# Kernel optimization log

Hardware: AMD Instinct MI355X
Metric: run time of the kernel (lower is better)

## Reference

```python
import jax, jax.numpy as jnp
import numpy as np

ATTENTION_DIM = 256
TEMPERATURE = 1.0
NEG_INF = -2.0**32 + 1.0  # matches tf code's padding value


def setup_inputs() -> dict:
    key = jax.random.key(0)
    k1, k2, k3, k4, k5, k6, k7 = jax.random.split(key, 7)
    B, Q, M, QD, MD, AD, VD = 8, 2048, 2048, 512, 512, 256, 256
    inputs = jax.random.normal(k1, (B, Q, QD), dtype=jnp.float32)
    memory = jax.random.normal(k2, (B, M, MD), dtype=jnp.float32)
    memory_lengths = jnp.maximum(jax.random.randint(k3, (B,), 0, M + 1), 1).astype(jnp.int32)
    query_lengths = jnp.maximum(jax.random.randint(k4, (B,), 0, Q + 1), 1).astype(jnp.int32)
    s = 0.02
    Wq = jax.random.normal(k5, (QD, AD), dtype=jnp.float32) * s
    Wk = jax.random.normal(k6, (MD, AD), dtype=jnp.float32) * s
    Wv = jax.random.normal(k7, (MD, VD), dtype=jnp.float32) * s
    return {"inputs": inputs, "memory": memory, "memory_lengths": memory_lengths,
            "query_lengths": query_lengths, "Wq": Wq, "Wk": Wk, "Wv": Wv}


def reference(inputs, memory, memory_lengths, query_lengths, Wq, Wk, Wv):
    # Dense projections (no bias). NOTE: original code (faithfully reproduced)
    # computes values with the KEY layer; Wv is unused.
    queries = jnp.einsum('bqd,da->bqa', inputs, Wq)   # [B,Q,AD]
    keys = jnp.einsum('bmd,da->bma', memory, Wk)      # [B,M,AD]
    values = jnp.einsum('bmd,da->bma', memory, Wk)    # [B,M,AD] (bug in source)

    logits = jnp.einsum('bqa,bma->bqm', queries, keys)
    logits = logits / jnp.sqrt(jnp.float32(ATTENTION_DIM)) / TEMPERATURE

    B, Q, _ = inputs.shape
    M = memory.shape[1]
    mem_mask = jnp.arange(M)[None, :] < memory_lengths[:, None]   # [B,M]
    qry_mask = jnp.arange(Q)[None, :] < query_lengths[:, None]    # [B,Q]
    length_mask = qry_mask[:, :, None] & mem_mask[:, None, :]     # [B,Q,M]

    logits = jnp.where(length_mask, logits, jnp.float32(NEG_INF))
    alignments = jax.nn.softmax(logits, axis=2)                   # [B,Q,M]
    contexts = jnp.einsum('bqm,bma->bqa', alignments, values)     # [B,Q,AD]
    return contexts, alignments
```

## Files before the change

### kernel.cpp

```cpp
#include <hip/hip_runtime.h>
#include <hip/hip_bf16.h>

typedef __attribute__((ext_vector_type(8))) short s8v;
typedef __attribute__((ext_vector_type(4))) float f4v;
typedef __attribute__((ext_vector_type(4))) unsigned short us4;
typedef unsigned short u16;

__device__ __forceinline__ u16 f2bf(float f) {
  union { float f; unsigned int u; } x;
  x.f = f;
  unsigned int lsb = (x.u >> 16) & 1u;
  return (u16)((x.u + 0x7fffu + lsb) >> 16);
}

__device__ __forceinline__ uint4 pack8(float4 a, float4 b) {
  union { u16 u[8]; uint4 v; } t;
  t.u[0] = f2bf(a.x); t.u[1] = f2bf(a.y); t.u[2] = f2bf(a.z); t.u[3] = f2bf(a.w);
  t.u[4] = f2bf(b.x); t.u[5] = f2bf(b.y); t.u[6] = f2bf(b.z); t.u[7] = f2bf(b.w);
  return t.v;
}

__global__ __launch_bounds__(256) void proj_kernel(
    const float* __restrict__ inputs, const float* __restrict__ memory,
    const float* __restrict__ Wq, const float* __restrict__ Wk,
    u16* __restrict__ qb, u16* __restrict__ krow, u16* __restrict__ kcol)
{
  __shared__ u16 Wt[64 * 264];
  __shared__ u16 At[64 * 40];

  const int tid = threadIdx.x;
  const int w = tid >> 6;
  const int l = tid & 63;
  const int lr = l & 15;
  const int lh = l >> 4;
  const int rbase = blockIdx.x * 64;
  const int n0 = blockIdx.y * 64;
  const int src = blockIdx.z;
  const float* __restrict__ A  = src ? memory : inputs;
  const float* __restrict__ Wg = src ? Wk : Wq;

  f4v acc[4];
#pragma unroll
  for (int i = 0; i < 4; ++i) acc[i] = f4v{0.f, 0.f, 0.f, 0.f};

  for (int kh = 0; kh < 2; ++kh) {
    {
      const int kl = tid >> 3;
      const int nl = (tid & 7) * 8;
#pragma unroll
      for (int i = 0; i < 8; ++i) {
        const int k = kl + i * 32;
        const float* s = Wg + (size_t)(kh * 256 + k) * 256 + n0 + nl;
        float4 x0 = *(const float4*)s;
        float4 x1 = *(const float4*)(s + 4);
        Wt[(nl + 0) * 264 + k] = f2bf(x0.x);
        Wt[(nl + 1) * 264 + k] = f2bf(x0.y);
        Wt[(nl + 2) * 264 + k] = f2bf(x0.z);
        Wt[(nl + 3) * 264 + k] = f2bf(x0.w);
        Wt[(nl + 4) * 264 + k] = f2bf(x1.x);
        Wt[(nl + 5) * 264 + k] = f2bf(x1.y);
        Wt[(nl + 6) * 264 + k] = f2bf(x1.z);
        Wt[(nl + 7) * 264 + k] = f2bf(x1.w);
      }
    }
    __syncthreads();
    for (int ks = 0; ks < 8; ++ks) {
      {
        const int row = tid >> 2;
        const int kk = (tid & 3) * 8;
        const float* s = A + (size_t)(rbase + row) * 512 + kh * 256 + ks * 32 + kk;
        float4 x0 = *(const float4*)s;
        float4 x1 = *(const float4*)(s + 4);
        *(uint4*)&At[row * 40 + kk] = pack8(x0, x1);
      }
      __syncthreads();
      const s8v af = *(const s8v*)&At[(w * 16 + lr) * 40 + lh * 8];
#pragma unroll
      for (int nt = 0; nt < 4; ++nt) {
        const s8v bf = *(const s8v*)&Wt[(nt * 16 + lr) * 264 + ks * 32 + lh * 8];
        acc[nt] = __builtin_amdgcn_mfma_f32_16x16x32_bf16(af, bf, acc[nt], 0, 0, 0);
      }
      __syncthreads();
    }
  }

  u16* __restrict__ dst = src ? krow : qb;
#pragma unroll
  for (int nt = 0; nt < 4; ++nt) {
    const int col = n0 + nt * 16 + lr;
    const int R0 = rbase + w * 16 + lh * 4;
    u16 u0 = f2bf(acc[nt][0]);
    u16 u1 = f2bf(acc[nt][1]);
    u16 u2 = f2bf(acc[nt][2]);
    u16 u3 = f2bf(acc[nt][3]);
    dst[(size_t)(R0 + 0) * 256 + col] = u0;
    dst[(size_t)(R0 + 1) * 256 + col] = u1;
    dst[(size_t)(R0 + 2) * 256 + col] = u2;
    dst[(size_t)(R0 + 3) * 256 + col] = u3;
    if (src) {
      const int bb = R0 >> 11;
      const int mm = R0 & 2047;
      us4 pk;
      pk[0] = u0; pk[1] = u1; pk[2] = u2; pk[3] = u3;
      *(us4*)&kcol[((size_t)bb * 256 + col) * 2048 + mm] = pk;
    }
  }
}

__global__ __launch_bounds__(256) void attn_sum_kernel(
    const u16* __restrict__ qb, const u16* __restrict__ krow,
    const int* __restrict__ mlens, const int* __restrict__ qlens,
    float* __restrict__ psum_p)
{
  __shared__ u16 kr[32 * 264];

  const int tid = threadIdx.x;
  const int w = tid >> 6;
  const int l = tid & 63;
  const int lr = l & 15;
  const int lh = l >> 4;
  const int bid = blockIdx.x;
  const int b = bid & 7;
  const int q0 = ((bid >> 3) & 31) * 64;
  const int ms = bid >> 8;
  const int m_base = ms * 256;
  const int mlen = mlens[b];
  const int qlen = qlens[b];
  const int qrow0 = q0 + w * 16 + lh * 4;

  s8v qf[8];
  {
    const u16* qp = qb + ((size_t)b * 2048 + q0 + w * 16 + lr) * 256 + lh * 8;
#pragma unroll
    for (int s = 0; s < 8; ++s) qf[s] = *(const s8v*)(qp + s * 32);
  }

  float psum[4] = {0.f, 0.f, 0.f, 0.f};
  const float C2 = 0.09016844005556021f;

  for (int mo = 0; mo < 256; mo += 32) {
    const int m0 = m_base + mo;
#pragma unroll
    for (int i = 0; i < 4; ++i) {
      const int idx = i * 256 + tid;
      const int m = idx >> 5, G = idx & 31;
      uint4 v = *(const uint4*)(krow + (((size_t)b * 2048 + m0 + m) << 8) + G * 8);
      *(uint4*)&kr[m * 264 + G * 8] = v;
    }
    __syncthreads();

    f4v sacc[2];
    sacc[0] = f4v{0.f, 0.f, 0.f, 0.f};
    sacc[1] = f4v{0.f, 0.f, 0.f, 0.f};
#pragma unroll
    for (int s = 0; s < 8; ++s) {
#pragma unroll
      for (int f = 0; f < 2; ++f) {
        const s8v bf = *(const s8v*)&kr[(f * 16 + lr) * 264 + s * 32 + lh * 8];
        sacc[f] = __builtin_amdgcn_mfma_f32_16x16x32_bf16(qf[s], bf, sacc[f], 0, 0, 0);
      }
    }
#pragma unroll
    for (int f = 0; f < 2; ++f) {
      const int m = m0 + f * 16 + lr;
      const bool vm = m < mlen;
#pragma unroll
      for (int r = 0; r < 4; ++r) {
        float p = exp2f(sacc[f][r] * C2);
        if (!vm) p = 0.f;
        if (qrow0 + r >= qlen) p = 1.f;
        psum[r] += p;
      }
    }
    __syncthreads();
  }

#pragma unroll
  for (int r = 0; r < 4; ++r) {
    float v = psum[r];
    v += __shfl_xor(v, 1);
    v += __shfl_xor(v, 2);
    v += __shfl_xor(v, 4);
    v += __shfl_xor(v, 8);
    psum[r] = v;
  }
  if (lr == 0) {
#pragma unroll
    for (int r = 0; r < 4; ++r)
      psum_p[ms * 16384 + b * 2048 + qrow0 + r] = psum[r];
  }
}

__global__ __launch_bounds__(256) void attn_wr_kernel(
    const u16* __restrict__ qb, const u16* __restrict__ krow,
    const u16* __restrict__ kcol, const int* __restrict__ mlens,
    const int* __restrict__ qlens, const float* __restrict__ psum_p,
    float* __restrict__ out_align, float* __restrict__ out_ctx,
    float* __restrict__ octx_ws)
{
  __shared__ u16 kr[32 * 264];
  __shared__ u16 kc[256 * 40];
  __shared__ u16 pl[4 * 16 * 40];

  const int tid = threadIdx.x;
  const int w = tid >> 6;
  const int l = tid & 63;
  const int lr = l & 15;
  const int lh = l >> 4;
  const int bid = blockIdx.x;
  const int b = bid & 7;
  const int q0 = ((bid >> 3) & 31) * 64;
  const int mh = bid >> 8;
  const int mstart = (mh == 0) ? 0 : (mh == 1 ? 704 : 1376);
  const int ntile = (mh == 0) ? 22 : 21;
  const int mlen = mlens[b];
  const int qlen = qlens[b];
  const int qrow0 = q0 + w * 16 + lh * 4;

  s8v qf[8];
  {
    const u16* qp = qb + ((size_t)b * 2048 + q0 + w * 16 + lr) * 256 + lh * 8;
#pragma unroll
    for (int s = 0; s < 8; ++s) qf[s] = *(const s8v*)(qp + s * 32);
  }

  float inv[4];
#pragma unroll
  for (int r = 0; r < 4; ++r) {
    const int q = b * 2048 + qrow0 + r;
    float s = 0.f;
#pragma unroll
    for (int j = 0; j < 8; ++j) s += psum_p[j * 16384 + q];
    inv[r] = 1.0f / s;
  }

  f4v oacc[16];
#pragma unroll
  for (int i = 0; i < 16; ++i) oacc[i] = f4v{0.f, 0.f, 0.f, 0.f};

  const float C2 = 0.09016844005556021f;

  for (int t = 0; t < ntile; ++t) {
    const int m0 = mstart + t * 32;
#pragma unroll
    for (int i = 0; i < 4; ++i) {
      const int idx = i * 256 + tid;
      const int m = idx >> 5, G = idx & 31;
      uint4 v = *(const uint4*)(krow + (((size_t)b * 2048 + m0 + m) << 8) + G * 8);
      *(uint4*)&kr[m * 264 + G * 8] = v;
      const int a2 = idx >> 2, gm = idx & 3;
      uint4 v2 = *(const uint4*)(kcol + (((size_t)b * 256 + a2) << 11) + m0 + gm * 8);
      *(uint4*)&kc[a2 * 40 + gm * 8] = v2;
    }
    __syncthreads();

    f4v sacc[2];
    sacc[0] = f4v{0.f, 0.f, 0.f, 0.f};
    sacc[1] = f4v{0.f, 0.f, 0.f, 0.f};
#pragma unroll
    for (int s = 0; s < 8; ++s) {
#pragma unroll
      for (int f = 0; f < 2; ++f) {
        const s8v bf = *(const s8v*)&kr[(f * 16 + lr) * 264 + s * 32 + lh * 8];
        sacc[f] = __builtin_amdgcn_mfma_f32_16x16x32_bf16(qf[s], bf, sacc[f], 0, 0, 0);
      }
    }

#pragma unroll
    for (int f = 0; f < 2; ++f) {
      const int m = m0 + f * 16 + lr;
      const bool vm = m < mlen;
#pragma unroll
      for (int r = 0; r < 4; ++r) {
        const int q = qrow0 + r;
        float p = exp2f(sacc[f][r] * C2);
        if (!vm) p = 0.f;
        if (q >= qlen) p = 1.f;
        const float pn = p * inv[r];
        __builtin_nontemporal_store(pn, &out_align[((size_t)b * 2048 + q) * 2048 + m]);
        pl[w * 640 + (lh * 4 + r) * 40 + f * 16 + lr] = f2bf(pn);
      }
    }

    const s8v pa = *(const s8v*)&pl[w * 640 + lr * 40 + lh * 8];
#pragma unroll
    for (int at = 0; at < 16; ++at) {
      const s8v vf = *(const s8v*)&kc[(at * 16 + lr) * 40 + lh * 8];
      oacc[at] = __builtin_amdgcn_mfma_f32_16x16x32_bf16(pa, vf, oacc[at], 0, 0, 0);
    }
    __syncthreads();
  }

  float* __restrict__ dst = (mh == 0) ? out_ctx : (octx_ws + (size_t)(mh - 1) * 4194304);
#pragma unroll
  for (int at = 0; at < 16; ++at) {
    const int a = at * 16 + lr;
#pragma unroll
    for (int r = 0; r < 4; ++r) {
      __builtin_nontemporal_store(oacc[at][r],
          &dst[((size_t)b * 2048 + qrow0 + r) * 256 + a]);
    }
  }
}

__global__ __launch_bounds__(256) void combine_kernel(
    float* __restrict__ out_ctx, const float* __restrict__ octx_ws)
{
  const size_t i = (size_t)blockIdx.x * 256 + threadIdx.x;
  float4 a = ((const float4*)out_ctx)[i];
  float4 c0 = ((const float4*)octx_ws)[i];
  float4 c1 = ((const float4*)(octx_ws + 4194304))[i];
  a.x += c0.x + c1.x; a.y += c0.y + c1.y;
  a.z += c0.z + c1.z; a.w += c0.w + c1.w;
  ((float4*)out_ctx)[i] = a;
}

extern "C" void kernel_launch(void* const* d_in, const int* in_sizes, int n_in,
                              void* d_out, int out_size, void* d_ws, size_t ws_size,
                              hipStream_t stream) {
  const float* inputs = (const float*)d_in[0];
  const float* memory = (const float*)d_in[1];
  const int* mlens    = (const int*)d_in[2];
  const int* qlens    = (const int*)d_in[3];
  const float* Wq     = (const float*)d_in[4];
  const float* Wk     = (const float*)d_in[5];
  (void)in_sizes; (void)n_in; (void)out_size; (void)ws_size;

  u16* wsu = (u16*)d_ws;
  u16* qb   = wsu;
  u16* krow = wsu + 4194304;
  u16* kcol = wsu + 8388608;
  float* psum_p = (float*)(wsu + 12582912);
  float* octx_ws = (float*)(wsu + 12845056);

  float* out_ctx = (float*)d_out;
  float* out_align = out_ctx + 4194304;

  proj_kernel<<<dim3(256, 4, 2), dim3(256), 0, stream>>>(
      inputs, memory, Wq, Wk, qb, krow, kcol);
  attn_sum_kernel<<<dim3(2048), dim3(256), 0, stream>>>(
      qb, krow, mlens, qlens, psum_p);
  attn_wr_kernel<<<dim3(768), dim3(256), 0, stream>>>(
      qb, krow, kcol, mlens, qlens, psum_p, out_align, out_ctx, octx_ws);
  combine_kernel<<<dim3(4096), dim3(256), 0, stream>>>(out_ctx, octx_ws);
}
```

Before: 187.5 us.

## Process two query tiles per block to reuse staged K tiles

Both attention kernels now give each block 128 query rows, as two 64-row sub-tiles, so every K tile staged in LDS serves twice the queries. This halves the global-to-LDS traffic for K. The write kernel also changes its memory split from three uneven chunks to four equal 512-column chunks. The combine kernel therefore sums three partial context buffers instead of two. The cost is doubled register state per thread (Q fragments and output accumulators), which may lower occupancy, plus a larger workspace and more reduction traffic in combine.

After: 254.9 us. +35.9%, slower.

```diff
diff --git a/kernel.cpp b/kernel.cpp
--- a/kernel.cpp
+++ b/kernel.cpp
@@ -121,21 +121,25 @@
   const int lh = l >> 4;
   const int bid = blockIdx.x;
   const int b = bid & 7;
-  const int q0 = ((bid >> 3) & 31) * 64;
-  const int ms = bid >> 8;
+  const int q0 = ((bid >> 3) & 15) * 128;
+  const int ms = bid >> 7;
   const int m_base = ms * 256;
   const int mlen = mlens[b];
   const int qlen = qlens[b];
-  const int qrow0 = q0 + w * 16 + lh * 4;
-
-  s8v qf[8];
-  {
-    const u16* qp = qb + ((size_t)b * 2048 + q0 + w * 16 + lr) * 256 + lh * 8;
-#pragma unroll
-    for (int s = 0; s < 8; ++s) qf[s] = *(const s8v*)(qp + s * 32);
-  }
-
-  float psum[4] = {0.f, 0.f, 0.f, 0.f};
+
+  s8v qf[2][8];
+#pragma unroll
+  for (int qt = 0; qt < 2; ++qt) {
+    const u16* qp = qb + ((size_t)b * 2048 + q0 + qt * 64 + w * 16 + lr) * 256 + lh * 8;
+#pragma unroll
+    for (int s = 0; s < 8; ++s) qf[qt][s] = *(const s8v*)(qp + s * 32);
+  }
+
+  float psum[2][4];
+#pragma unroll
+  for (int qt = 0; qt < 2; ++qt)
+#pragma unroll
+    for (int r = 0; r < 4; ++r) psum[qt][r] = 0.f;
   const float C2 = 0.09016844005556021f;
 
   for (int mo = 0; mo < 256; mo += 32) {
@@ -149,45 +153,53 @@
     }
     __syncthreads();
 
-    f4v sacc[2];
-    sacc[0] = f4v{0.f, 0.f, 0.f, 0.f};
-    sacc[1] = f4v{0.f, 0.f, 0.f, 0.f};
-#pragma unroll
-    for (int s = 0; s < 8; ++s) {
+#pragma unroll
+    for (int qt = 0; qt < 2; ++qt) {
+      f4v sacc[2];
+      sacc[0] = f4v{0.f, 0.f, 0.f, 0.f};
+      sacc[1] = f4v{0.f, 0.f, 0.f, 0.f};
+#pragma unroll
+      for (int s = 0; s < 8; ++s) {
+#pragma unroll
+        for (int f = 0; f < 2; ++f) {
+          const s8v bf = *(const s8v*)&kr[(f * 16 + lr) * 264 + s * 32 + lh * 8];
+          sacc[f] = __builtin_amdgcn_mfma_f32_16x16x32_bf16(qf[qt][s], bf, sacc[f], 0, 0, 0);
+        }
+      }
+      const int qrow0 = q0 + qt * 64 + w * 16 + lh * 4;
 #pragma unroll
       for (int f = 0; f < 2; ++f) {
-        const s8v bf = *(const s8v*)&kr[(f * 16 + lr) * 264 + s * 32 + lh * 8];
-        sacc[f] = __builtin_amdgcn_mfma_f32_16x16x32_bf16(qf[s], bf, sacc[f], 0, 0, 0);
-      }
-    }
-#pragma unroll
-    for (int f = 0; f < 2; ++f) {
-      const int m = m0 + f * 16 + lr;
-      const bool vm = m < mlen;
-#pragma unroll
-      for (int r = 0; r < 4; ++r) {
-        float p = exp2f(sacc[f][r] * C2);
-        if (!vm) p = 0.f;
-        if (qrow0 + r >= qlen) p = 1.f;
-        psum[r] += p;
-      }
-    }
-    __syncthreads();
-  }
-
-#pragma unroll
-  for (int r = 0; r < 4; ++r) {
-    float v = psum[r];
-    v += __shfl_xor(v, 1);
-    v += __shfl_xor(v, 2);
-    v += __shfl_xor(v, 4);
-    v += __shfl_xor(v, 8);
-    psum[r] = v;
-  }
-  if (lr == 0) {
-#pragma unroll
-    for (int r = 0; r < 4; ++r)
-      psum_p[ms * 16384 + b * 2048 + qrow0 + r] = psum[r];
+        const int m = m0 + f * 16 + lr;
+        const bool vm = m < mlen;
+#pragma unroll
+        for (int r = 0; r < 4; ++r) {
+          float p = exp2f(sacc[f][r] * C2);
+          if (!vm) p = 0.f;
+          if (qrow0 + r >= qlen) p = 1.f;
+          psum[qt][r] += p;
+        }
+      }
+    }
+    __syncthreads();
+  }
+
+#pragma unroll
+  for (int qt = 0; qt < 2; ++qt) {
+#pragma unroll
+    for (int r = 0; r < 4; ++r) {
+      float v = psum[qt][r];
+      v += __shfl_xor(v, 1);
+      v += __shfl_xor(v, 2);
+      v += __shfl_xor(v, 4);
+      v += __shfl_xor(v, 8);
+      psum[qt][r] = v;
+    }
+    if (lr == 0) {
+      const int qrow0 = q0 + qt * 64 + w * 16 + lh * 4;
+#pragma unroll
+      for (int r = 0; r < 4; ++r)
+        psum_p[ms * 16384 + b * 2048 + qrow0 + r] = psum[qt][r];
+    }
   }
 }
 
@@ -209,39 +221,43 @@
   const int lh = l >> 4;
   const int bid = blockIdx.x;
   const int b = bid & 7;
-  const int q0 = ((bid >> 3) & 31) * 64;
-  const int mh = bid >> 8;
-  const int mstart = (mh == 0) ? 0 : (mh == 1 ? 704 : 1376);
-  const int ntile = (mh == 0) ? 22 : 21;
+  const int q0 = ((bid >> 3) & 15) * 128;
+  const int mh = bid >> 7;
+  const int m_base = mh * 512;
   const int mlen = mlens[b];
   const int qlen = qlens[b];
-  const int qrow0 = q0 + w * 16 + lh * 4;
-
-  s8v qf[8];
-  {
-    const u16* qp = qb + ((size_t)b * 2048 + q0 + w * 16 + lr) * 256 + lh * 8;
-#pragma unroll
-    for (int s = 0; s < 8; ++s) qf[s] = *(const s8v*)(qp + s * 32);
-  }
-
-  float inv[4];
-#pragma unroll
-  for (int r = 0; r < 4; ++r) {
-    const int q = b * 2048 + qrow0 + r;
-    float s = 0.f;
-#pragma unroll
-    for (int j = 0; j < 8; ++j) s += psum_p[j * 16384 + q];
-    inv[r] = 1.0f / s;
-  }
-
-  f4v oacc[16];
-#pragma unroll
-  for (int i = 0; i < 16; ++i) oacc[i] = f4v{0.f, 0.f, 0.f, 0.f};
+
+  s8v qf[2][8];
+#pragma unroll
+  for (int qt = 0; qt < 2; ++qt) {
+    const u16* qp = qb + ((size_t)b * 2048 + q0 + qt * 64 + w * 16 + lr) * 256 + lh * 8;
+#pragma unroll
+    for (int s = 0; s < 8; ++s) qf[qt][s] = *(const s8v*)(qp + s * 32);
+  }
+
+  float inv[2][4];
+#pragma unroll
+  for (int qt = 0; qt < 2; ++qt) {
+#pragma unroll
+    for (int r = 0; r < 4; ++r) {
+      const int q = b * 2048 + q0 + qt * 64 + w * 16 + lh * 4 + r;
+      float s = 0.f;
+#pragma unroll
+      for (int j = 0; j < 8; ++j) s += psum_p[j * 16384 + q];
+      inv[qt][r] = 1.0f / s;
+    }
+  }
+
+  f4v oacc[2][16];
+#pragma unroll
+  for (int qt = 0; qt < 2; ++qt)
+#pragma unroll
+    for (int i = 0; i < 16; ++i) oacc[qt][i] = f4v{0.f, 0.f, 0.f, 0.f};
 
   const float C2 = 0.09016844005556021f;
 
-  for (int t = 0; t < ntile; ++t) {
-    const int m0 = mstart + t * 32;
+  for (int mo = 0; mo < 512; mo += 32) {
+    const int m0 = m_base + mo;
 #pragma unroll
     for (int i = 0; i < 4; ++i) {
       const int idx = i * 256 + tid;
@@ -254,51 +270,59 @@
     }
     __syncthreads();
 
-    f4v sacc[2];
-    sacc[0] = f4v{0.f, 0.f, 0.f, 0.f};
-    sacc[1] = f4v{0.f, 0.f, 0.f, 0.f};
-#pragma unroll
-    for (int s = 0; s < 8; ++s) {
+#pragma unroll
+    for (int qt = 0; qt < 2; ++qt) {
+      f4v sacc[2];
+      sacc[0] = f4v{0.f, 0.f, 0.f, 0.f};
+      sacc[1] = f4v{0.f, 0.f, 0.f, 0.f};
+#pragma unroll
+      for (int s = 0; s < 8; ++s) {
+#pragma unroll
+        for (int f = 0; f < 2; ++f) {
+          const s8v bf = *(const s8v*)&kr[(f * 16 + lr) * 264 + s * 32 + lh * 8];
+          sacc[f] = __builtin_amdgcn_mfma_f32_16x16x32_bf16(qf[qt][s], bf, sacc[f], 0, 0, 0);
+        }
+      }
+
+      const int qrow0 = q0 + qt * 64 + w * 16 + lh * 4;
 #pragma unroll
       for (int f = 0; f < 2; ++f) {
-        const s8v bf = *(const s8v*)&kr[(f * 16 + lr) * 264 + s * 32 + lh * 8];
-        sacc[f] = __builtin_amdgcn_mfma_f32_16x16x32_bf16(qf[s], bf, sacc[f], 0, 0, 0);
-      }
-    }
-
-#pragma unroll
-    for (int f = 0; f < 2; ++f) {
-      const int m = m0 + f * 16 + lr;
-      const bool vm = m < mlen;
+        const int m = m0 + f * 16 + lr;
+        const bool vm = m < mlen;
+#pragma unroll
+        for (int r = 0; r < 4; ++r) {
+          const int q = qrow0 + r;
+          float p = exp2f(sacc[f][r] * C2);
+          if (!vm) p = 0.f;
+          if (q >= qlen) p = 1.f;
+          const float pn = p * inv[qt][r];
+          __builtin_nontemporal_store(pn, &out_align[((size_t)b * 2048 + q) * 2048 + m]);
+          pl[w * 640 + (lh * 4 + r) * 40 + f * 16 + lr] = f2bf(pn);
+        }
+      }
+
+      const s8v pa = *(const s8v*)&pl[w * 640 + lr * 40 + lh * 8];
+#pragma unroll
+      for (int at = 0; at < 16; ++at) {
+        const s8v vf = *(const s8v*)&kc[(at * 16 + lr) * 40 + lh * 8];
+        oacc[qt][at] = __builtin_amdgcn_mfma_f32_16x16x32_bf16(pa, vf, oacc[qt][at], 0, 0, 0);
+      }
+    }
+    __syncthreads();
+  }
+
+  float* __restrict__ dst = (mh == 0) ? out_ctx : (octx_ws + (size_t)(mh - 1) * 4194304);
+#pragma unroll
+  for (int qt = 0; qt < 2; ++qt) {
+    const int qrow0 = q0 + qt * 64 + w * 16 + lh * 4;
+#pragma unroll
+    for (int at = 0; at < 16; ++at) {
+      const int a = at * 16 + lr;
 #pragma unroll
       for (int r = 0; r < 4; ++r) {
-        const int q = qrow0 + r;
-        float p = exp2f(sacc[f][r] * C2);
-        if (!vm) p = 0.f;
-        if (q >= qlen) p = 1.f;
-        const float pn = p * inv[r];
-        __builtin_nontemporal_store(pn, &out_align[((size_t)b * 2048 + q) * 2048 + m]);
-        pl[w * 640 + (lh * 4 + r) * 40 + f * 16 + lr] = f2bf(pn);
-      }
-    }
-
-    const s8v pa = *(const s8v*)&pl[w * 640 + lr * 40 + lh * 8];
-#pragma unroll
-    for (int at = 0; at < 16; ++at) {
-      const s8v vf = *(const s8v*)&kc[(at * 16 + lr) * 40 + lh * 8];
-      oacc[at] = __builtin_amdgcn_mfma_f32_16x16x32_bf16(pa, vf, oacc[at], 0, 0, 0);
-    }
-    __syncthreads();
-  }
-
-  float* __restrict__ dst = (mh == 0) ? out_ctx : (octx_ws + (size_t)(mh - 1) * 4194304);
-#pragma unroll
-  for (int at = 0; at < 16; ++at) {
-    const int a = at * 16 + lr;
-#pragma unroll
-    for (int r = 0; r < 4; ++r) {
-      __builtin_nontemporal_store(oacc[at][r],
-          &dst[((size_t)b * 2048 + qrow0 + r) * 256 + a]);
+        __builtin_nontemporal_store(oacc[qt][at][r],
+            &dst[((size_t)b * 2048 + qrow0 + r) * 256 + a]);
+      }
     }
   }
 }
@@ -310,8 +334,11 @@
   float4 a = ((const float4*)out_ctx)[i];
   float4 c0 = ((const float4*)octx_ws)[i];
   float4 c1 = ((const float4*)(octx_ws + 4194304))[i];
-  a.x += c0.x + c1.x; a.y += c0.y + c1.y;
-  a.z += c0.z + c1.z; a.w += c0.w + c1.w;
+  float4 c2 = ((const float4*)(octx_ws + 8388608))[i];
+  a.x += c0.x + c1.x + c2.x;
+  a.y += c0.y + c1.y + c2.y;
+  a.z += c0.z + c1.z + c2.z;
+  a.w += c0.w + c1.w + c2.w;
   ((float4*)out_ctx)[i] = a;
 }
 
@@ -338,9 +365,9 @@
 
   proj_kernel<<<dim3(256, 4, 2), dim3(256), 0, stream>>>(
       inputs, memory, Wq, Wk, qb, krow, kcol);
-  attn_sum_kernel<<<dim3(2048), dim3(256), 0, stream>>>(
+  attn_sum_kernel<<<dim3(1024), dim3(256), 0, stream>>>(
       qb, krow, mlens, qlens, psum_p);
-  attn_wr_kernel<<<dim3(768), dim3(256), 0, stream>>>(
+  attn_wr_kernel<<<dim3(512), dim3(256), 0, stream>>>(
       qb, krow, kcol, mlens, qlens, psum_p, out_align, out_ctx, octx_ws);
   combine_kernel<<<dim3(4096), dim3(256), 0, stream>>>(out_ctx, octx_ws);
 }
```

## Switch attention kernels to 32x32x16 MFMA with 128-row query tiles

Applied to the files above, without the earlier changes.

Both attention kernels now use 32x32x16 bf16 MFMA, so each wave covers 32 query rows instead of 16. The intent is more reuse of each LDS fragment and fewer LDS reads per MFMA. The key dimension in the write kernel is split into four 512-wide chunks instead of three uneven ones, and the combine kernel sums an extra partial context buffer. The trade-offs are more registers per thread (launch bounds now ask for 2 blocks), fewer blocks in flight, and extra workspace and combine traffic.

Result: slower. 231.0 us (+23.2%).

```diff
diff --git a/kernel.cpp b/kernel.cpp
--- a/kernel.cpp
+++ b/kernel.cpp
@@ -3,6 +3,7 @@
 
 typedef __attribute__((ext_vector_type(8))) short s8v;
 typedef __attribute__((ext_vector_type(4))) float f4v;
+typedef __attribute__((ext_vector_type(16))) float f16v;
 typedef __attribute__((ext_vector_type(4))) unsigned short us4;
 typedef unsigned short u16;
 
@@ -117,25 +118,27 @@
   const int tid = threadIdx.x;
   const int w = tid >> 6;
   const int l = tid & 63;
-  const int lr = l & 15;
-  const int lh = l >> 4;
+  const int lm = l & 31;
+  const int lk = l >> 5;
   const int bid = blockIdx.x;
   const int b = bid & 7;
-  const int q0 = ((bid >> 3) & 31) * 64;
-  const int ms = bid >> 8;
+  const int q0 = ((bid >> 3) & 15) * 128;
+  const int ms = bid >> 7;
   const int m_base = ms * 256;
   const int mlen = mlens[b];
   const int qlen = qlens[b];
-  const int qrow0 = q0 + w * 16 + lh * 4;
-
-  s8v qf[8];
+  const int q0w = q0 + w * 32;
+
+  s8v qf[16];
   {
-    const u16* qp = qb + ((size_t)b * 2048 + q0 + w * 16 + lr) * 256 + lh * 8;
-#pragma unroll
-    for (int s = 0; s < 8; ++s) qf[s] = *(const s8v*)(qp + s * 32);
-  }
-
-  float psum[4] = {0.f, 0.f, 0.f, 0.f};
+    const u16* qp = qb + ((size_t)b * 2048 + q0w + lm) * 256 + lk * 8;
+#pragma unroll
+    for (int c = 0; c < 16; ++c) qf[c] = *(const s8v*)(qp + c * 16);
+  }
+
+  float psum[16];
+#pragma unroll
+  for (int i = 0; i < 16; ++i) psum[i] = 0.f;
   const float C2 = 0.09016844005556021f;
 
   for (int mo = 0; mo < 256; mo += 32) {
@@ -149,49 +152,48 @@
     }
     __syncthreads();
 
-    f4v sacc[2];
-    sacc[0] = f4v{0.f, 0.f, 0.f, 0.f};
-    sacc[1] = f4v{0.f, 0.f, 0.f, 0.f};
-#pragma unroll
-    for (int s = 0; s < 8; ++s) {
-#pragma unroll
-      for (int f = 0; f < 2; ++f) {
-        const s8v bf = *(const s8v*)&kr[(f * 16 + lr) * 264 + s * 32 + lh * 8];
-        sacc[f] = __builtin_amdgcn_mfma_f32_16x16x32_bf16(qf[s], bf, sacc[f], 0, 0, 0);
-      }
-    }
-#pragma unroll
-    for (int f = 0; f < 2; ++f) {
-      const int m = m0 + f * 16 + lr;
-      const bool vm = m < mlen;
-#pragma unroll
-      for (int r = 0; r < 4; ++r) {
-        float p = exp2f(sacc[f][r] * C2);
-        if (!vm) p = 0.f;
-        if (qrow0 + r >= qlen) p = 1.f;
-        psum[r] += p;
-      }
-    }
-    __syncthreads();
-  }
-
-#pragma unroll
-  for (int r = 0; r < 4; ++r) {
-    float v = psum[r];
+    f16v sacc;
+#pragma unroll
+    for (int i = 0; i < 16; ++i) sacc[i] = 0.f;
+#pragma unroll
+    for (int c = 0; c < 16; ++c) {
+      const s8v bf = *(const s8v*)&kr[lm * 264 + c * 16 + lk * 8];
+      sacc = __builtin_amdgcn_mfma_f32_32x32x16_bf16(qf[c], bf, sacc, 0, 0, 0);
+    }
+
+    const int m = m0 + lm;
+    const bool vm = m < mlen;
+#pragma unroll
+    for (int reg = 0; reg < 16; ++reg) {
+      const int q = q0w + (reg & 3) + 8 * (reg >> 2) + 4 * lk;
+      float p = exp2f(sacc[reg] * C2);
+      if (!vm) p = 0.f;
+      if (q >= qlen) p = 1.f;
+      psum[reg] += p;
+    }
+    __syncthreads();
+  }
+
+#pragma unroll
+  for (int reg = 0; reg < 16; ++reg) {
+    float v = psum[reg];
     v += __shfl_xor(v, 1);
     v += __shfl_xor(v, 2);
     v += __shfl_xor(v, 4);
     v += __shfl_xor(v, 8);
-    psum[r] = v;
-  }
-  if (lr == 0) {
-#pragma unroll
-    for (int r = 0; r < 4; ++r)
-      psum_p[ms * 16384 + b * 2048 + qrow0 + r] = psum[r];
-  }
-}
-
-__global__ __launch_bounds__(256) void attn_wr_kernel(
+    v += __shfl_xor(v, 16);
+    psum[reg] = v;
+  }
+  if (lm == 0) {
+#pragma unroll
+    for (int reg = 0; reg < 16; ++reg) {
+      const int q = q0w + (reg & 3) + 8 * (reg >> 2) + 4 * lk;
+      psum_p[ms * 16384 + b * 2048 + q] = psum[reg];
+    }
+  }
+}
+
+__global__ __launch_bounds__(256, 2) void attn_wr_kernel(
     const u16* __restrict__ qb, const u16* __restrict__ krow,
     const u16* __restrict__ kcol, const int* __restrict__ mlens,
     const int* __restrict__ qlens, const float* __restrict__ psum_p,
@@ -200,48 +202,49 @@
 {
   __shared__ u16 kr[32 * 264];
   __shared__ u16 kc[256 * 40];
-  __shared__ u16 pl[4 * 16 * 40];
+  __shared__ u16 pl[4 * 32 * 40];
 
   const int tid = threadIdx.x;
   const int w = tid >> 6;
   const int l = tid & 63;
-  const int lr = l & 15;
-  const int lh = l >> 4;
+  const int lm = l & 31;
+  const int lk = l >> 5;
   const int bid = blockIdx.x;
   const int b = bid & 7;
-  const int q0 = ((bid >> 3) & 31) * 64;
-  const int mh = bid >> 8;
-  const int mstart = (mh == 0) ? 0 : (mh == 1 ? 704 : 1376);
-  const int ntile = (mh == 0) ? 22 : 21;
+  const int q0 = ((bid >> 3) & 15) * 128;
+  const int mh = bid >> 7;
+  const int m_base = mh * 512;
   const int mlen = mlens[b];
   const int qlen = qlens[b];
-  const int qrow0 = q0 + w * 16 + lh * 4;
-
-  s8v qf[8];
+  const int q0w = q0 + w * 32;
+
+  s8v qf[16];
   {
-    const u16* qp = qb + ((size_t)b * 2048 + q0 + w * 16 + lr) * 256 + lh * 8;
-#pragma unroll
-    for (int s = 0; s < 8; ++s) qf[s] = *(const s8v*)(qp + s * 32);
-  }
-
-  float inv[4];
-#pragma unroll
-  for (int r = 0; r < 4; ++r) {
-    const int q = b * 2048 + qrow0 + r;
+    const u16* qp = qb + ((size_t)b * 2048 + q0w + lm) * 256 + lk * 8;
+#pragma unroll
+    for (int c = 0; c < 16; ++c) qf[c] = *(const s8v*)(qp + c * 16);
+  }
+
+  float inv[16];
+#pragma unroll
+  for (int reg = 0; reg < 16; ++reg) {
+    const int q = b * 2048 + q0w + (reg & 3) + 8 * (reg >> 2) + 4 * lk;
     float s = 0.f;
 #pragma unroll
     for (int j = 0; j < 8; ++j) s += psum_p[j * 16384 + q];
-    inv[r] = 1.0f / s;
-  }
-
-  f4v oacc[16];
-#pragma unroll
-  for (int i = 0; i < 16; ++i) oacc[i] = f4v{0.f, 0.f, 0.f, 0.f};
+    inv[reg] = 1.0f / s;
+  }
+
+  f16v oacc[8];
+#pragma unroll
+  for (int at = 0; at < 8; ++at)
+#pragma unroll
+    for (int i = 0; i < 16; ++i) oacc[at][i] = 0.f;
 
   const float C2 = 0.09016844005556021f;
 
-  for (int t = 0; t < ntile; ++t) {
-    const int m0 = mstart + t * 32;
+  for (int mo = 0; mo < 512; mo += 32) {
+    const int m0 = m_base + mo;
 #pragma unroll
     for (int i = 0; i < 4; ++i) {
       const int idx = i * 256 + tid;
@@ -254,51 +257,50 @@
     }
     __syncthreads();
 
-    f4v sacc[2];
-    sacc[0] = f4v{0.f, 0.f, 0.f, 0.f};
-    sacc[1] = f4v{0.f, 0.f, 0.f, 0.f};
-#pragma unroll
-    for (int s = 0; s < 8; ++s) {
-#pragma unroll
-      for (int f = 0; f < 2; ++f) {
-        const s8v bf = *(const s8v*)&kr[(f * 16 + lr) * 264 + s * 32 + lh * 8];
-        sacc[f] = __builtin_amdgcn_mfma_f32_16x16x32_bf16(qf[s], bf, sacc[f], 0, 0, 0);
-      }
-    }
-
-#pragma unroll
-    for (int f = 0; f < 2; ++f) {
-      const int m = m0 + f * 16 + lr;
-      const bool vm = m < mlen;
-#pragma unroll
-      for (int r = 0; r < 4; ++r) {
-        const int q = qrow0 + r;
-        float p = exp2f(sacc[f][r] * C2);
-        if (!vm) p = 0.f;
-        if (q >= qlen) p = 1.f;
-        const float pn = p * inv[r];
-        __builtin_nontemporal_store(pn, &out_align[((size_t)b * 2048 + q) * 2048 + m]);
-        pl[w * 640 + (lh * 4 + r) * 40 + f * 16 + lr] = f2bf(pn);
-      }
-    }
-
-    const s8v pa = *(const s8v*)&pl[w * 640 + lr * 40 + lh * 8];
-#pragma unroll
-    for (int at = 0; at < 16; ++at) {
-      const s8v vf = *(const s8v*)&kc[(at * 16 + lr) * 40 + lh * 8];
-      oacc[at] = __builtin_amdgcn_mfma_f32_16x16x32_bf16(pa, vf, oacc[at], 0, 0, 0);
+    f16v sacc;
+#pragma unroll
+    for (int i = 0; i < 16; ++i) sacc[i] = 0.f;
+#pragma unroll
+    for (int c = 0; c < 16; ++c) {
+      const s8v bf = *(const s8v*)&kr[lm * 264 + c * 16 + lk * 8];
+      sacc = __builtin_amdgcn_mfma_f32_32x32x16_bf16(qf[c], bf, sacc, 0, 0, 0);
+    }
+
+    const int m = m0 + lm;
+    const bool vm = m < mlen;
+#pragma unroll
+    for (int reg = 0; reg < 16; ++reg) {
+      const int qloc = (reg & 3) + 8 * (reg >> 2) + 4 * lk;
+      const int q = q0w + qloc;
+      float p = exp2f(sacc[reg] * C2);
+      if (!vm) p = 0.f;
+      if (q >= qlen) p = 1.f;
+      const float pn = p * inv[reg];
+      __builtin_nontemporal_store(pn, &out_align[((size_t)b * 2048 + q) * 2048 + m]);
+      pl[w * 1280 + qloc * 40 + lm] = f2bf(pn);
+    }
+
+    s8v pa0 = *(const s8v*)&pl[w * 1280 + lm * 40 + lk * 8];
+    s8v pa1 = *(const s8v*)&pl[w * 1280 + lm * 40 + 16 + lk * 8];
+#pragma unroll
+    for (int at = 0; at < 8; ++at) {
+      const s8v vf0 = *(const s8v*)&kc[(at * 32 + lm) * 40 + lk * 8];
+      oacc[at] = __builtin_amdgcn_mfma_f32_32x32x16_bf16(pa0, vf0, oacc[at], 0, 0, 0);
+      const s8v vf1 = *(const s8v*)&kc[(at * 32 + lm) * 40 + 16 + lk * 8];
+      oacc[at] = __builtin_amdgcn_mfma_f32_32x32x16_bf16(pa1, vf1, oacc[at], 0, 0, 0);
     }
     __syncthreads();
   }
 
   float* __restrict__ dst = (mh == 0) ? out_ctx : (octx_ws + (size_t)(mh - 1) * 4194304);
 #pragma unroll
-  for (int at = 0; at < 16; ++at) {
-    const int a = at * 16 + lr;
-#pragma unroll
-    for (int r = 0; r < 4; ++r) {
-      __builtin_nontemporal_store(oacc[at][r],
-          &dst[((size_t)b * 2048 + qrow0 + r) * 256 + a]);
+  for (int at = 0; at < 8; ++at) {
+    const int a = at * 32 + lm;
+#pragma unroll
+    for (int reg = 0; reg < 16; ++reg) {
+      const int q = q0w + (reg & 3) + 8 * (reg >> 2) + 4 * lk;
+      __builtin_nontemporal_store(oacc[at][reg],
+          &dst[((size_t)b * 2048 + q) * 256 + a]);
     }
   }
 }
@@ -310,8 +312,11 @@
   float4 a = ((const float4*)out_ctx)[i];
   float4 c0 = ((const float4*)octx_ws)[i];
   float4 c1 = ((const float4*)(octx_ws + 4194304))[i];
-  a.x += c0.x + c1.x; a.y += c0.y + c1.y;
-  a.z += c0.z + c1.z; a.w += c0.w + c1.w;
+  float4 c2 = ((const float4*)(octx_ws + 8388608))[i];
+  a.x += c0.x + c1.x + c2.x;
+  a.y += c0.y + c1.y + c2.y;
+  a.z += c0.z + c1.z + c2.z;
+  a.w += c0.w + c1.w + c2.w;
   ((float4*)out_ctx)[i] = a;
 }
 
@@ -338,9 +343,9 @@
 
   proj_kernel<<<dim3(256, 4, 2), dim3(256), 0, stream>>>(
       inputs, memory, Wq, Wk, qb, krow, kcol);
-  attn_sum_kernel<<<dim3(2048), dim3(256), 0, stream>>>(
+  attn_sum_kernel<<<dim3(1024), dim3(256), 0, stream>>>(
       qb, krow, mlens, qlens, psum_p);
-  attn_wr_kernel<<<dim3(768), dim3(256), 0, stream>>>(
+  attn_wr_kernel<<<dim3(512), dim3(256), 0, stream>>>(
       qb, krow, kcol, mlens, qlens, psum_p, out_align, out_ctx, octx_ws);
   combine_kernel<<<dim3(4096), dim3(256), 0, stream>>>(out_ctx, octx_ws);
 }
```
